# Kernel optimization log

Hardware: AMD Instinct MI355X
Metric: run time of the kernel (lower is better)

The kernel has to match this reference:

```python
import jax, jax.numpy as jnp
import numpy as np

ALIGN_CORNERS = False  # matches init_kwargs


def setup_inputs() -> dict:
    key = jax.random.key(0)
    k1, k2 = jax.random.split(key)
    features = jax.random.normal(k1, (8, 128, 128, 256), dtype=jnp.float32)
    grid = jax.random.uniform(k2, (8, 16384, 2), dtype=jnp.float32)  # values in [0, 1)
    return {"features": features, "grid": grid}


def reference(features, grid):
    # features: [B, H, W, C] (NHWC), grid: [B, P, 2] with values in [0, 1], last axis (x, y)
    B, H, W, C = features.shape
    # pad H and W by 1 on each side so out-of-range corner taps read zeros
    safe = jnp.pad(features, ((0, 0), (1, 1), (1, 1), (0, 0))).astype(grid.dtype)

    g = grid[..., ::-1]  # reverse last axis -> (y, x) matching (H, W)
    size = jnp.asarray([H, W], dtype=grid.dtype)
    if ALIGN_CORNERS:
        g = g * (size - 1)
    else:
        g = (2.0 * g * size - 1.0) / 2.0

    bounds = jnp.asarray([H + 1, W + 1], dtype=jnp.int32)  # per-axis clip max in padded map
    batch_idx = jnp.arange(B)[:, None]  # [B, 1], broadcasts over P

    def lookup(coords):
        c = jnp.clip(coords.astype(jnp.int32) + 1, 0, bounds)  # shift into padded coords
        return safe[batch_idx, c[..., 0], c[..., 1]]  # [B, P, C]

    g_nw = jnp.floor(g)
    g_ne = g_nw + jnp.asarray([1.0, 0.0], g.dtype)
    g_sw = g_nw + jnp.asarray([0.0, 1.0], g.dtype)
    g_se = g_nw + jnp.asarray([1.0, 1.0], g.dtype)

    one = jnp.asarray([1.0, -1.0], g.dtype)
    w_nw = jnp.prod(g_se - g, axis=-1, keepdims=True)
    w_ne = jnp.prod((g_sw - g) * one, axis=-1, keepdims=True)
    w_sw = jnp.prod((g_ne - g) * -one, axis=-1, keepdims=True)
    w_se = jnp.prod(g - g_nw, axis=-1, keepdims=True)

    result = (lookup(g_nw) * w_nw + lookup(g_ne) * w_ne
              + lookup(g_sw) * w_sw + lookup(g_se) * w_se)
    return result.astype(features.dtype)  # [B, P, C]
```

## Files before the change

### kernel.cpp

```cpp
#include <hip/hip_runtime.h>


constexpr int B = 8, H = 128, W = 128, C = 256, P = 16384;
constexpr int PPW = 4;
constexpr int TS = 32;
constexpr int TPS = W / TS;
constexpr int TPB = TPS * TPS;
constexpr int NT = B * TPB;
constexpr int NPTS = B * P;
constexpr int NBLK = NPTS / (4 * PPW);

typedef float f32x4 __attribute__((ext_vector_type(4)));

__device__ __forceinline__ int tile_of(int pt, const float* grid) {
    const int b = pt >> 14;
    const float2 g = reinterpret_cast<const float2*>(grid)[pt];
    int ix = (int)floorf(g.x * (float)W - 0.5f);
    int iy = (int)floorf(g.y * (float)H - 0.5f);
    ix = min(max(ix, 0), W - 1);
    iy = min(max(iy, 0), H - 1);
    return b * TPB + (iy / TS) * TPS + (ix / TS);
}

__global__ __launch_bounds__(256) void histo_kernel(
    const float* __restrict__ grid, int* __restrict__ cnt)
{
    __shared__ int h[NT];
    const int tid = threadIdx.x;
    for (int i = tid; i < NT; i += 256) h[i] = 0;
    __syncthreads();
    const int pt = blockIdx.x * 256 + tid;
    atomicAdd(&h[tile_of(pt, grid)], 1);
    __syncthreads();
    for (int i = tid; i < NT; i += 256) if (h[i]) atomicAdd(&cnt[i], h[i]);
}

__global__ __launch_bounds__(NT) void scan_kernel(
    const int* __restrict__ cnt, int* __restrict__ cur)
{
    __shared__ int s[NT];
    const int tid = threadIdx.x;
    const int v0 = cnt[tid];
    s[tid] = v0;
    __syncthreads();
    for (int off = 1; off < NT; off <<= 1) {
        int v = 0;
        if (tid >= off) v = s[tid - off];
        __syncthreads();
        s[tid] += v;
        __syncthreads();
    }
    cur[tid] = s[tid] - v0;
}

__global__ __launch_bounds__(256) void scatter_kernel(
    const float* __restrict__ grid, int* __restrict__ cur, int* __restrict__ perm)
{
    __shared__ int h[NT];
    __shared__ int base[NT];
    const int tid = threadIdx.x;
    for (int i = tid; i < NT; i += 256) h[i] = 0;
    __syncthreads();
    const int pt = blockIdx.x * 256 + tid;
    const int t = tile_of(pt, grid);
    const int rank = atomicAdd(&h[t], 1);
    __syncthreads();
    for (int i = tid; i < NT; i += 256)
        base[i] = h[i] ? atomicAdd(&cur[i], h[i]) : 0;
    __syncthreads();
    perm[base[t] + rank] = pt;
}

__global__ __launch_bounds__(256) void point_sample_kernel(
    const float* __restrict__ features,
    const float* __restrict__ grid,
    const int* __restrict__ perm,
    float* __restrict__ out)
{
    const int wave = threadIdx.x >> 6;
    const int lane = threadIdx.x & 63;
    int bid = blockIdx.x;
    bid = (bid & 7) * (NBLK >> 3) + (bid >> 3);
    const int w = bid * 4 + wave;

    const int4 pv = *reinterpret_cast<const int4*>(perm + w * PPW);
    const int ptv[PPW] = {pv.x, pv.y, pv.z, pv.w};
    const int c = lane * 4;

    int   off[PPW][4];
    float wgt[PPW][4];
    #pragma unroll
    for (int k = 0; k < PPW; ++k) {
        const int pt = ptv[k];
        const int b = pt >> 14;
        const float2 g = reinterpret_cast<const float2*>(grid)[pt];
        const float x = g.x * (float)W - 0.5f;
        const float y = g.y * (float)H - 0.5f;
        const float fx = floorf(x), fy = floorf(y);
        const int ix = (int)fx, iy = (int)fy;
        const float frx = x - fx, fry = y - fy;

        const int x0 = min(max(ix, 0), W - 1);
        const int x1 = min(max(ix + 1, 0), W - 1);
        const int y0 = min(max(iy, 0), H - 1);
        const int y1 = min(max(iy + 1, 0), H - 1);
        const float mx0 = (ix >= 0 && ix < W)         ? 1.f : 0.f;
        const float mx1 = (ix + 1 >= 0 && ix + 1 < W) ? 1.f : 0.f;
        const float my0 = (iy >= 0 && iy < H)         ? 1.f : 0.f;
        const float my1 = (iy + 1 >= 0 && iy + 1 < H) ? 1.f : 0.f;

        wgt[k][0] = (1.f - fry) * (1.f - frx) * my0 * mx0;
        wgt[k][1] = (1.f - fry) * frx         * my0 * mx1;
        wgt[k][2] = fry         * (1.f - frx) * my1 * mx0;
        wgt[k][3] = fry         * frx         * my1 * mx1;
        const int fbase = b * (H * W * C) + c;
        off[k][0] = fbase + (y0 * W + x0) * C;
        off[k][1] = fbase + (y0 * W + x1) * C;
        off[k][2] = fbase + (y1 * W + x0) * C;
        off[k][3] = fbase + (y1 * W + x1) * C;
    }

    float4 v[PPW][4];
    #pragma unroll
    for (int k = 0; k < PPW; ++k)
        #pragma unroll
        for (int j = 0; j < 4; ++j)
            v[k][j] = *reinterpret_cast<const float4*>(features + off[k][j]);

    #pragma unroll
    for (int k = 0; k < PPW; ++k) {
        f32x4 acc = (f32x4)0.f;
        #pragma unroll
        for (int j = 0; j < 4; ++j) {
            const float wq = wgt[k][j];
            acc.x += wq * v[k][j].x;
            acc.y += wq * v[k][j].y;
            acc.z += wq * v[k][j].z;
            acc.w += wq * v[k][j].w;
        }
        f32x4* op = reinterpret_cast<f32x4*>(out + (size_t)ptv[k] * C + c);
        __builtin_nontemporal_store(acc, op);
    }
}

__global__ __launch_bounds__(256) void point_sample_direct(
    const float* __restrict__ features,
    const float* __restrict__ grid,
    float* __restrict__ out)
{
    const int wave = threadIdx.x >> 6;
    const int lane = threadIdx.x & 63;
    const int pt = blockIdx.x * 4 + wave;
    const int b = pt >> 14;
    const float2 g = reinterpret_cast<const float2*>(grid)[pt];
    const float x = g.x * (float)W - 0.5f;
    const float y = g.y * (float)H - 0.5f;
    const float fx = floorf(x), fy = floorf(y);
    const int ix = (int)fx, iy = (int)fy;
    const float frx = x - fx, fry = y - fy;
    const float* fb = features + (size_t)b * H * W * C;
    const int c = lane * 4;
    f32x4 acc = (f32x4)0.f;
    #pragma unroll
    for (int dy = 0; dy < 2; ++dy) {
        const int hy = iy + dy;
        const bool vy = (hy >= 0) && (hy < H);
        #pragma unroll
        for (int dx = 0; dx < 2; ++dx) {
            const int wx = ix + dx;
            if (vy && (wx >= 0) && (wx < W)) {
                const float wgt = dy ? (dx ? fry * frx : fry * (1.f - frx))
                                     : (dx ? (1.f - fry) * frx : (1.f - fry) * (1.f - frx));
                const float4 vv = *reinterpret_cast<const float4*>(
                    fb + ((size_t)hy * W + wx) * C + c);
                acc.x += wgt * vv.x; acc.y += wgt * vv.y;
                acc.z += wgt * vv.z; acc.w += wgt * vv.w;
            }
        }
    }
    f32x4* op = reinterpret_cast<f32x4*>(out + (size_t)pt * C + c);
    __builtin_nontemporal_store(acc, op);
}

extern "C" void kernel_launch(void* const* d_in, const int* in_sizes, int n_in,
                              void* d_out, int out_size, void* d_ws, size_t ws_size,
                              hipStream_t stream) {
    const float* features = (const float*)d_in[0];
    const float* grid     = (const float*)d_in[1];
    float* out            = (float*)d_out;

    const size_t need = (size_t)(2 * NT + NPTS) * sizeof(int);
    if (ws_size < need) {
        point_sample_direct<<<NPTS / 4, 256, 0, stream>>>(features, grid, out);
        return;
    }

    int* cnt  = (int*)d_ws;
    int* cur  = cnt + NT;
    int* perm = cur + NT;

    hipMemsetAsync(cnt, 0, NT * sizeof(int), stream);
    histo_kernel  <<<NPTS / 256, 256, 0, stream>>>(grid, cnt);
    scan_kernel   <<<1, NT, 0, stream>>>(cnt, cur);
    scatter_kernel<<<NPTS / 256, 256, 0, stream>>>(grid, cur, perm);
    point_sample_kernel<<<NBLK, 256, 0, stream>>>(features, grid, perm, out);
}
```

Measured before the change: 56.62 us.

## Fuse prefix scan into scatter kernel and process two points per thread

Removes the separate single-block scan kernel. Each scatter block now recomputes the exclusive prefix over tile counts in shared memory and adds a per-tile atomic offset from a second zeroed array. Histogram and scatter threads each handle two points through a float4 grid load, which halves the block count. This cuts one kernel launch and its serialization, at the cost of redundant scans across blocks and an extra memset region.

After: 54.13 us. -4.4%, faster.

```diff
diff --git a/kernel.cpp b/kernel.cpp
--- a/kernel.cpp
+++ b/kernel.cpp
@@ -12,11 +12,9 @@
 
 typedef float f32x4 __attribute__((ext_vector_type(4)));
 
-__device__ __forceinline__ int tile_of(int pt, const float* grid) {
-    const int b = pt >> 14;
-    const float2 g = reinterpret_cast<const float2*>(grid)[pt];
-    int ix = (int)floorf(g.x * (float)W - 0.5f);
-    int iy = (int)floorf(g.y * (float)H - 0.5f);
+__device__ __forceinline__ int tile_of_xy(int b, float gx, float gy) {
+    int ix = (int)floorf(gx * (float)W - 0.5f);
+    int iy = (int)floorf(gy * (float)H - 0.5f);
     ix = min(max(ix, 0), W - 1);
     iy = min(max(iy, 0), H - 1);
     return b * TPB + (iy / TS) * TPS + (ix / TS);
@@ -27,48 +25,53 @@
 {
     __shared__ int h[NT];
     const int tid = threadIdx.x;
-    for (int i = tid; i < NT; i += 256) h[i] = 0;
-    __syncthreads();
-    const int pt = blockIdx.x * 256 + tid;
-    atomicAdd(&h[tile_of(pt, grid)], 1);
-    __syncthreads();
-    for (int i = tid; i < NT; i += 256) if (h[i]) atomicAdd(&cnt[i], h[i]);
-}
-
-__global__ __launch_bounds__(NT) void scan_kernel(
-    const int* __restrict__ cnt, int* __restrict__ cur)
-{
-    __shared__ int s[NT];
+    if (tid < NT) h[tid] = 0;
+    __syncthreads();
+    const int pt0 = (blockIdx.x * 256 + tid) * 2;
+    const float4 g = *reinterpret_cast<const float4*>(grid + (size_t)pt0 * 2);
+    const int b = pt0 >> 14;
+    atomicAdd(&h[tile_of_xy(b, g.x, g.y)], 1);
+    atomicAdd(&h[tile_of_xy(b, g.z, g.w)], 1);
+    __syncthreads();
+    if (tid < NT && h[tid]) atomicAdd(&cnt[tid], h[tid]);
+}
+
+__global__ __launch_bounds__(256) void scatter_kernel(
+    const float* __restrict__ grid, const int* __restrict__ cnt,
+    int* __restrict__ off0, int* __restrict__ perm)
+{
+    __shared__ int h[NT];
+    __shared__ int pre[NT];
+    __shared__ int base[NT];
     const int tid = threadIdx.x;
-    const int v0 = cnt[tid];
-    s[tid] = v0;
-    __syncthreads();
+    int cv = 0;
+    if (tid < NT) { h[tid] = 0; cv = cnt[tid]; pre[tid] = cv; }
+    __syncthreads();
+
+    const int pt0 = (blockIdx.x * 256 + tid) * 2;
+    const float4 g = *reinterpret_cast<const float4*>(grid + (size_t)pt0 * 2);
+    const int b = pt0 >> 14;
+    const int t0 = tile_of_xy(b, g.x, g.y);
+    const int t1 = tile_of_xy(b, g.z, g.w);
+    const int r0 = atomicAdd(&h[t0], 1);
+    const int r1 = atomicAdd(&h[t1], 1);
+
+    #pragma unroll
     for (int off = 1; off < NT; off <<= 1) {
         int v = 0;
-        if (tid >= off) v = s[tid - off];
+        if (tid < NT && tid >= off) v = pre[tid - off];
         __syncthreads();
-        s[tid] += v;
+        if (tid < NT) pre[tid] += v;
         __syncthreads();
     }
-    cur[tid] = s[tid] - v0;
-}
-
-__global__ __launch_bounds__(256) void scatter_kernel(
-    const float* __restrict__ grid, int* __restrict__ cur, int* __restrict__ perm)
-{
-    __shared__ int h[NT];
-    __shared__ int base[NT];
-    const int tid = threadIdx.x;
-    for (int i = tid; i < NT; i += 256) h[i] = 0;
-    __syncthreads();
-    const int pt = blockIdx.x * 256 + tid;
-    const int t = tile_of(pt, grid);
-    const int rank = atomicAdd(&h[t], 1);
-    __syncthreads();
-    for (int i = tid; i < NT; i += 256)
-        base[i] = h[i] ? atomicAdd(&cur[i], h[i]) : 0;
-    __syncthreads();
-    perm[base[t] + rank] = pt;
+
+    if (tid < NT) {
+        const int hh = h[tid];
+        base[tid] = (pre[tid] - cv) + (hh ? atomicAdd(&off0[tid], hh) : 0);
+    }
+    __syncthreads();
+    perm[base[t0] + r0] = pt0;
+    perm[base[t1] + r1] = pt0 + 1;
 }
 
 __global__ __launch_bounds__(256) void point_sample_kernel(
@@ -196,12 +199,11 @@
     }
 
     int* cnt  = (int*)d_ws;
-    int* cur  = cnt + NT;
-    int* perm = cur + NT;
-
-    hipMemsetAsync(cnt, 0, NT * sizeof(int), stream);
-    histo_kernel  <<<NPTS / 256, 256, 0, stream>>>(grid, cnt);
-    scan_kernel   <<<1, NT, 0, stream>>>(cnt, cur);
-    scatter_kernel<<<NPTS / 256, 256, 0, stream>>>(grid, cur, perm);
+    int* off0 = cnt + NT;
+    int* perm = off0 + NT;
+
+    hipMemsetAsync(cnt, 0, 2 * NT * sizeof(int), stream);
+    histo_kernel  <<<NPTS / 512, 256, 0, stream>>>(grid, cnt);
+    scatter_kernel<<<NPTS / 512, 256, 0, stream>>>(grid, cnt, off0, perm);
     point_sample_kernel<<<NBLK, 256, 0, stream>>>(features, grid, perm, out);
 }
```
